# Optimization experiments

Measured on AMD Instinct MI355X. Metric: run time of the kernel, lower is better.

Reference implementation:

```python
import jax, jax.numpy as jnp
import numpy as np

M, P, B, TLEN = 512, 256, 128, 1024

def setup_inputs() -> dict:
    key = jax.random.key(0)
    k1, k2, k3, k4, k5, k6 = jax.random.split(key, 6)
    d_t = jax.random.normal(k1, (1, B, P), dtype=jnp.float32)
    s_t = jax.random.normal(k2, (1, B, P), dtype=jnp.float32)
    H = jax.random.normal(k3, (B, TLEN, M), dtype=jnp.float32)
    # torch.nn.Linear weights: shape [out_features, in_features]
    W_d = jax.random.normal(k4, (M, 2 * P), dtype=jnp.float32) / np.sqrt(2 * P)
    U_d = jax.random.normal(k5, (M, M), dtype=jnp.float32) / np.sqrt(M)
    v_d = jax.random.normal(k6, (1, M), dtype=jnp.float32) / np.sqrt(M)
    return {"d_t": d_t, "s_t": s_t, "H": H, "T": TLEN, "W_d": W_d, "U_d": U_d, "v_d": v_d}

def reference(d_t, s_t, H, T, W_d, U_d, v_d):
    # query: cat([d_t, s_t], dim=2) -> [1, B, 2p]; permute(1,0,2) -> [B, 1, 2p]
    query = jnp.concatenate([d_t, s_t], axis=2).transpose(1, 0, 2)  # [B, 1, 2p]
    # W_d(query) broadcast over T instead of materializing the repeat (same math)
    wq = jnp.einsum('boc,mc->bom', query, W_d)          # [B, 1, m]
    uh = jnp.einsum('btm,nm->btn', H, U_d)              # [B, T, m]
    beta = jnp.tanh(wq + uh)                            # [B, T, m]
    score = jnp.einsum('btm,om->bto', beta, v_d)        # [B, T, 1]
    score = score.transpose(0, 2, 1)                    # [B, 1, T]
    return jax.nn.softmax(score, axis=2)
```

## Files before the change

### kernel.cpp

```cpp
#include <hip/hip_runtime.h>
#include <hip/hip_bf16.h>
#include <stdint.h>

#define NB   128
#define NT   1024
#define NM   512
#define NP   256

typedef __attribute__((ext_vector_type(8))) short bf16x8;
typedef __attribute__((ext_vector_type(4))) float f32x4;
typedef unsigned int u32;

__device__ __forceinline__ uint32_t bfpair(float a, float b) {
    uint32_t ua = __float_as_uint(a) + 0x8000u;
    uint32_t ub = __float_as_uint(b) + 0x8000u;
    return __builtin_amdgcn_perm(ub, ua, 0x07060302u);
}

__device__ __forceinline__ bf16x8 pack8(float4 lo, float4 hi) {
    union { bf16x8 v; uint32_t u[4]; } r;
    r.u[0] = bfpair(lo.x, lo.y);
    r.u[1] = bfpair(lo.z, lo.w);
    r.u[2] = bfpair(hi.x, hi.y);
    r.u[3] = bfpair(hi.z, hi.w);
    return r.v;
}

__device__ __forceinline__ float fast_tanh(float x) {
    float e = __expf(2.0f * x);
    return 1.0f - 2.0f * __builtin_amdgcn_rcpf(e + 1.0f);
}

typedef const __attribute__((address_space(1))) u32* gas_t;
typedef __attribute__((address_space(3))) u32* las_t;
__device__ __forceinline__ void dma16(const void* g, void* l) {
    __builtin_amdgcn_global_load_lds((gas_t)g, (las_t)l, 16, 0, 0);
}

__global__ void prep_kernel(const float* __restrict__ U, unsigned short* __restrict__ Ub,
                            const float* __restrict__ d_t, const float* __restrict__ s_t,
                            const float* __restrict__ W, float* __restrict__ wq,
                            float* __restrict__ out) {
    const int bx = blockIdx.x;
    if (bx < 256) {
        int idx = bx * 256 + threadIdx.x;
        float4 u = reinterpret_cast<const float4*>(U)[idx];
        reinterpret_cast<uint2*>(Ub)[idx] = make_uint2(bfpair(u.x, u.y), bfpair(u.z, u.w));
    } else if (bx < 384) {
        int g = (bx - 256) * 512 + threadIdx.x * 2;
        int b = g >> 9;
        const float* dt = d_t + (size_t)b * NP;
        const float* st = s_t + (size_t)b * NP;
        #pragma unroll
        for (int e = 0; e < 2; ++e) {
            int n = (g + e) & 511;
            const float* Wn = W + (size_t)n * 512;
            float s = 0.f;
            #pragma unroll 4
            for (int c = 0; c < NP; c += 4) {
                float4 w0 = *reinterpret_cast<const float4*>(Wn + c);
                float4 q0 = *reinterpret_cast<const float4*>(dt + c);
                s += w0.x * q0.x + w0.y * q0.y + w0.z * q0.z + w0.w * q0.w;
                float4 w1 = *reinterpret_cast<const float4*>(Wn + NP + c);
                float4 q1 = *reinterpret_cast<const float4*>(st + c);
                s += w1.x * q1.x + w1.y * q1.y + w1.z * q1.z + w1.w * q1.w;
            }
            wq[g + e] = s;
        }
    } else {
        int idx = (bx - 384) * 256 + threadIdx.x;
        reinterpret_cast<float4*>(out)[idx] = make_float4(0.f, 0.f, 0.f, 0.f);
    }
}

__global__ __launch_bounds__(256, 2)
void score_kernel(const float* __restrict__ H, const unsigned short* __restrict__ Ub,
                  const float* __restrict__ wq, const float* __restrict__ v_d,
                  float* __restrict__ out) {
    __shared__ float          As[2][128 * 32];
    __shared__ unsigned short Bs[2][256 * 32];
    __shared__ float s_score[128];

    const int tid  = threadIdx.x;
    const int id   = blockIdx.x;
    const int tile = (id >> 4) * 8 + (id & 7);
    const int nh   = (id >> 3) & 1;
    const int tt   = tile & 7;
    const int b    = tile >> 3;

    const int lane = tid & 63;
    const int w    = tid >> 6;
    const int lr   = lane & 15;
    const int lq   = lane >> 4;
    const int tw   = w >> 1;
    const int nw   = w & 1;

    if (tid < 128) s_score[tid] = 0.f;

    const float* gA[4];
    const unsigned short* gB[4];
    unsigned lL[4];
    #pragma unroll
    for (int q = 0; q < 4; ++q) {
        int rA = w * 32 + q * 8 + (lane >> 3);
        int cA = (lane & 7) ^ (rA & 7);
        gA[q] = H + ((size_t)(b * NT + tt * 128 + rA)) * NM + cA * 4;
        int rB = w * 64 + q * 16 + (lane >> 2);
        int cB = (lane & 3) ^ ((rB >> 1) & 3);
        gB[q] = Ub + ((size_t)(nh * 256 + rB)) * NM + cB * 8;
        lL[q] = (unsigned)((w * 4 + q) * 1024 + lane * 16);
    }

    f32x4 acc[4][8];
    #pragma unroll
    for (int i = 0; i < 4; ++i)
        #pragma unroll
        for (int j = 0; j < 8; ++j)
            acc[i][j] = (f32x4){0.f, 0.f, 0.f, 0.f};

    #pragma unroll
    for (int q = 0; q < 4; ++q) dma16(gA[q], (char*)As[0] + lL[q]);
    #pragma unroll
    for (int q = 0; q < 4; ++q) dma16(gB[q], (char*)Bs[0] + lL[q]);

    #pragma unroll
    for (int kk = 0; kk < 16; ++kk) {
        const int cur = kk & 1;
        const int nxt = cur ^ 1;
        __syncthreads();
        if (kk < 15) {
            #pragma unroll
            for (int q = 0; q < 4; ++q) { gA[q] += 32; dma16(gA[q], (char*)As[nxt] + lL[q]); }
            #pragma unroll
            for (int q = 0; q < 4; ++q) { gB[q] += 32; dma16(gB[q], (char*)Bs[nxt] + lL[q]); }
        }

        bf16x8 a[4];
        #pragma unroll
        for (int i = 0; i < 4; ++i) {
            int t_loc = tw * 64 + i * 16 + lr;
            int s = t_loc & 7;
            const char* base = (const char*)As[cur] + t_loc * 128;
            float4 lo = *reinterpret_cast<const float4*>(base + (((2 * lq)     ^ s) * 16));
            float4 hi = *reinterpret_cast<const float4*>(base + (((2 * lq + 1) ^ s) * 16));
            a[i] = pack8(lo, hi);
        }
        bf16x8 bb[8];
        #pragma unroll
        for (int j = 0; j < 8; ++j) {
            int n_loc = nw * 128 + j * 16 + lr;
            int slot = lq ^ ((n_loc >> 1) & 3);
            bb[j] = *reinterpret_cast<const bf16x8*>((const char*)Bs[cur] + n_loc * 64 + slot * 16);
        }

        #pragma unroll
        for (int i = 0; i < 4; ++i)
            #pragma unroll
            for (int j = 0; j < 8; ++j)
                acc[i][j] = __builtin_amdgcn_mfma_f32_16x16x32_bf16(a[i], bb[j], acc[i][j], 0, 0, 0);
    }

    const float* wqb = wq + (size_t)b * NM;
    float vv[8], wv[8];
    #pragma unroll
    for (int j = 0; j < 8; ++j) {
        int n = nh * 256 + nw * 128 + j * 16 + lr;
        vv[j] = v_d[n];
        wv[j] = wqb[n];
    }
    #pragma unroll
    for (int i = 0; i < 4; ++i) {
        #pragma unroll
        for (int r = 0; r < 4; ++r) {
            float s = 0.f;
            #pragma unroll
            for (int j = 0; j < 8; ++j)
                s += vv[j] * fast_tanh(wv[j] + acc[i][j][r]);
            #pragma unroll
            for (int off = 1; off < 16; off <<= 1)
                s += __shfl_xor(s, off, 64);
            if (lr == 0) atomicAdd(&s_score[tw * 64 + i * 16 + lq * 4 + r], s);
        }
    }
    __syncthreads();
    if (tid < 128) atomicAdd(&out[(size_t)b * NT + tt * 128 + tid], s_score[tid]);
}

__global__ void softmax_kernel(float* __restrict__ out) {
    const int b   = blockIdx.x;
    const int tid = threadIdx.x;
    float* p = out + (size_t)b * NT;
    float4 v = reinterpret_cast<float4*>(p)[tid];
    float m = fmaxf(fmaxf(v.x, v.y), fmaxf(v.z, v.w));
    #pragma unroll
    for (int off = 32; off >= 1; off >>= 1)
        m = fmaxf(m, __shfl_xor(m, off, 64));
    __shared__ float red[8];
    const int wv = tid >> 6;
    if ((tid & 63) == 0) red[wv] = m;
    __syncthreads();
    m = fmaxf(fmaxf(red[0], red[1]), fmaxf(red[2], red[3]));
    float e0 = __expf(v.x - m), e1 = __expf(v.y - m);
    float e2 = __expf(v.z - m), e3 = __expf(v.w - m);
    float s = e0 + e1 + e2 + e3;
    #pragma unroll
    for (int off = 32; off >= 1; off >>= 1)
        s += __shfl_xor(s, off, 64);
    if ((tid & 63) == 0) red[4 + wv] = s;
    __syncthreads();
    s = red[4] + red[5] + red[6] + red[7];
    float inv = 1.f / s;
    float4 o;
    o.x = e0 * inv; o.y = e1 * inv; o.z = e2 * inv; o.w = e3 * inv;
    reinterpret_cast<float4*>(p)[tid] = o;
}

extern "C" void kernel_launch(void* const* d_in, const int* in_sizes, int n_in,
                              void* d_out, int out_size, void* d_ws, size_t ws_size,
                              hipStream_t stream) {
    const float* d_t = (const float*)d_in[0];
    const float* s_t = (const float*)d_in[1];
    const float* H   = (const float*)d_in[2];
    const float* W_d = (const float*)d_in[4];
    const float* U_d = (const float*)d_in[5];
    const float* v_d = (const float*)d_in[6];
    float* out = (float*)d_out;

    unsigned short* Ub = (unsigned short*)d_ws;
    float* wq = (float*)((char*)d_ws + 512 * 1024);

    prep_kernel<<<512, 256, 0, stream>>>(U_d, Ub, d_t, s_t, W_d, wq, out);
    score_kernel<<<2048, 256, 0, stream>>>(H, Ub, wq, v_d, out);
    softmax_kernel<<<NB, 256, 0, stream>>>(out);
}
```

Before: 467.8 us.

## Convert H to bf16 at LDS store and triple-buffer U tiles

The H tile is now loaded into registers, converted to bf16 once and written to LDS, replacing the fp32 DMA path where every wave re-read fp32 and re-packed it per MFMA. This halves the A-tile LDS footprint and read traffic. U tiles use a three-stage ring with prefetch two steps ahead and hand-placed vmcnt/lgkmcnt waits plus raw barriers. The cost is more VGPRs for in-flight H values and fragile manual waitcnt ordering.

```diff
diff --git a/kernel.cpp b/kernel.cpp
--- a/kernel.cpp
+++ b/kernel.cpp
@@ -15,15 +15,6 @@
     uint32_t ua = __float_as_uint(a) + 0x8000u;
     uint32_t ub = __float_as_uint(b) + 0x8000u;
     return __builtin_amdgcn_perm(ub, ua, 0x07060302u);
-}
-
-__device__ __forceinline__ bf16x8 pack8(float4 lo, float4 hi) {
-    union { bf16x8 v; uint32_t u[4]; } r;
-    r.u[0] = bfpair(lo.x, lo.y);
-    r.u[1] = bfpair(lo.z, lo.w);
-    r.u[2] = bfpair(hi.x, hi.y);
-    r.u[3] = bfpair(hi.z, hi.w);
-    return r.v;
 }
 
 __device__ __forceinline__ float fast_tanh(float x) {
@@ -77,8 +68,8 @@
 void score_kernel(const float* __restrict__ H, const unsigned short* __restrict__ Ub,
                   const float* __restrict__ wq, const float* __restrict__ v_d,
                   float* __restrict__ out) {
-    __shared__ float          As[2][128 * 32];
-    __shared__ unsigned short Bs[2][256 * 32];
+    __shared__ unsigned short As[2][128 * 32];
+    __shared__ unsigned short Bs[3][256 * 32];
     __shared__ float s_score[128];
 
     const int tid  = threadIdx.x;
@@ -98,18 +89,24 @@
     if (tid < 128) s_score[tid] = 0.f;
 
     const float* gA[4];
+    u32 woff[4];
+    #pragma unroll
+    for (int q = 0; q < 4; ++q) {
+        int r = w * 32 + q * 8 + (lane >> 3);
+        gA[q] = H + ((size_t)(b * NT + tt * 128 + r)) * NM + (lane & 7) * 4;
+        woff[q] = (u32)(r * 64 + ((((lane & 7) >> 1) ^ ((r >> 1) & 3)) << 4) + (lane & 1) * 8);
+    }
     const unsigned short* gB[4];
-    unsigned lL[4];
+    u32 lB[4];
     #pragma unroll
     for (int q = 0; q < 4; ++q) {
-        int rA = w * 32 + q * 8 + (lane >> 3);
-        int cA = (lane & 7) ^ (rA & 7);
-        gA[q] = H + ((size_t)(b * NT + tt * 128 + rA)) * NM + cA * 4;
         int rB = w * 64 + q * 16 + (lane >> 2);
         int cB = (lane & 3) ^ ((rB >> 1) & 3);
         gB[q] = Ub + ((size_t)(nh * 256 + rB)) * NM + cB * 8;
-        lL[q] = (unsigned)((w * 4 + q) * 1024 + lane * 16);
-    }
+        lB[q] = (u32)((w * 4 + q) * 1024 + lane * 16);
+    }
+    const u32 aro = (u32)((tw * 64 + lr) * 64 + ((lq ^ ((lr >> 1) & 3)) << 4));
+    const u32 bro = (u32)((nw * 128 + lr) * 64 + ((lq ^ ((lr >> 1) & 3)) << 4));
 
     f32x4 acc[4][8];
     #pragma unroll
@@ -118,46 +115,68 @@
         for (int j = 0; j < 8; ++j)
             acc[i][j] = (f32x4){0.f, 0.f, 0.f, 0.f};
 
-    #pragma unroll
-    for (int q = 0; q < 4; ++q) dma16(gA[q], (char*)As[0] + lL[q]);
-    #pragma unroll
-    for (int q = 0; q < 4; ++q) dma16(gB[q], (char*)Bs[0] + lL[q]);
+    float4 av[4];
+    #pragma unroll
+    for (int q = 0; q < 4; ++q) { av[q] = *reinterpret_cast<const float4*>(gA[q]); gA[q] += 32; }
+    #pragma unroll
+    for (int q = 0; q < 4; ++q) { dma16(gB[q], (char*)Bs[0] + lB[q]); gB[q] += 32; }
+    #pragma unroll
+    for (int q = 0; q < 4; ++q)
+        *reinterpret_cast<uint2*>((char*)As[0] + woff[q]) =
+            make_uint2(bfpair(av[q].x, av[q].y), bfpair(av[q].z, av[q].w));
+    #pragma unroll
+    for (int q = 0; q < 4; ++q) { av[q] = *reinterpret_cast<const float4*>(gA[q]); gA[q] += 32; }
+    #pragma unroll
+    for (int q = 0; q < 4; ++q) { dma16(gB[q], (char*)Bs[1] + lB[q]); gB[q] += 32; }
+
+    asm volatile("s_waitcnt vmcnt(8)" ::: "memory");
+    asm volatile("s_waitcnt lgkmcnt(0)" ::: "memory");
+    __builtin_amdgcn_s_barrier();
+    __builtin_amdgcn_sched_barrier(0);
 
     #pragma unroll
     for (int kk = 0; kk < 16; ++kk) {
-        const int cur = kk & 1;
-        const int nxt = cur ^ 1;
-        __syncthreads();
+        const char* ab = (const char*)As[kk & 1] + aro;
+        bf16x8 a0 = *reinterpret_cast<const bf16x8*>(ab);
+        bf16x8 a1 = *reinterpret_cast<const bf16x8*>(ab + 1024);
+        bf16x8 a2 = *reinterpret_cast<const bf16x8*>(ab + 2048);
+        bf16x8 a3 = *reinterpret_cast<const bf16x8*>(ab + 3072);
+
         if (kk < 15) {
-            #pragma unroll
-            for (int q = 0; q < 4; ++q) { gA[q] += 32; dma16(gA[q], (char*)As[nxt] + lL[q]); }
-            #pragma unroll
-            for (int q = 0; q < 4; ++q) { gB[q] += 32; dma16(gB[q], (char*)Bs[nxt] + lL[q]); }
-        }
-
-        bf16x8 a[4];
-        #pragma unroll
-        for (int i = 0; i < 4; ++i) {
-            int t_loc = tw * 64 + i * 16 + lr;
-            int s = t_loc & 7;
-            const char* base = (const char*)As[cur] + t_loc * 128;
-            float4 lo = *reinterpret_cast<const float4*>(base + (((2 * lq)     ^ s) * 16));
-            float4 hi = *reinterpret_cast<const float4*>(base + (((2 * lq + 1) ^ s) * 16));
-            a[i] = pack8(lo, hi);
-        }
-        bf16x8 bb[8];
+            char* an = (char*)As[(kk + 1) & 1];
+            #pragma unroll
+            for (int q = 0; q < 4; ++q)
+                *reinterpret_cast<uint2*>(an + woff[q]) =
+                    make_uint2(bfpair(av[q].x, av[q].y), bfpair(av[q].z, av[q].w));
+        }
+        if (kk < 14) {
+            #pragma unroll
+            for (int q = 0; q < 4; ++q) { av[q] = *reinterpret_cast<const float4*>(gA[q]); gA[q] += 32; }
+            char* bn = (char*)Bs[(kk + 2) % 3];
+            #pragma unroll
+            for (int q = 0; q < 4; ++q) { dma16(gB[q], bn + lB[q]); gB[q] += 32; }
+        }
+
+        const char* bbb = (const char*)Bs[kk % 3] + bro;
         #pragma unroll
         for (int j = 0; j < 8; ++j) {
-            int n_loc = nw * 128 + j * 16 + lr;
-            int slot = lq ^ ((n_loc >> 1) & 3);
-            bb[j] = *reinterpret_cast<const bf16x8*>((const char*)Bs[cur] + n_loc * 64 + slot * 16);
-        }
-
-        #pragma unroll
-        for (int i = 0; i < 4; ++i)
-            #pragma unroll
-            for (int j = 0; j < 8; ++j)
-                acc[i][j] = __builtin_amdgcn_mfma_f32_16x16x32_bf16(a[i], bb[j], acc[i][j], 0, 0, 0);
+            bf16x8 bbj = *reinterpret_cast<const bf16x8*>(bbb + j * 1024);
+            acc[0][j] = __builtin_amdgcn_mfma_f32_16x16x32_bf16(a0, bbj, acc[0][j], 0, 0, 0);
+            acc[1][j] = __builtin_amdgcn_mfma_f32_16x16x32_bf16(a1, bbj, acc[1][j], 0, 0, 0);
+            acc[2][j] = __builtin_amdgcn_mfma_f32_16x16x32_bf16(a2, bbj, acc[2][j], 0, 0, 0);
+            acc[3][j] = __builtin_amdgcn_mfma_f32_16x16x32_bf16(a3, bbj, acc[3][j], 0, 0, 0);
+        }
+
+        if (kk < 14) {
+            asm volatile("s_waitcnt vmcnt(8)" ::: "memory");
+        } else if (kk == 14) {
+            asm volatile("s_waitcnt vmcnt(0)" ::: "memory");
+        }
+        if (kk < 15) {
+            asm volatile("s_waitcnt lgkmcnt(0)" ::: "memory");
+            __builtin_amdgcn_s_barrier();
+            __builtin_amdgcn_sched_barrier(0);
+        }
     }
 
     const float* wqb = wq + (size_t)b * NM;
```

Measured after the change: 455.4 us. 2.7% less time.

## Restructure score kernel as persistent per-batch loop with register-resident U weights

Applied to the files above, without the earlier changes.

Each block now owns one batch and one half of the output features, keeping its slice of the bf16 U matrix in registers and looping over all time tiles. H is loaded into registers, converted to bf16 with a packed convert instruction, and written into a double-buffered LDS tile, with one barrier per k-step. This removes repeated U tile loads and per-use fp32-to-bf16 packing from LDS. In exchange it uses fewer, larger blocks with heavy register use, which risks low occupancy and latency exposure.

```diff
diff --git a/kernel.cpp b/kernel.cpp
--- a/kernel.cpp
+++ b/kernel.cpp
@@ -17,24 +17,15 @@
     return __builtin_amdgcn_perm(ub, ua, 0x07060302u);
 }
 
-__device__ __forceinline__ bf16x8 pack8(float4 lo, float4 hi) {
-    union { bf16x8 v; uint32_t u[4]; } r;
-    r.u[0] = bfpair(lo.x, lo.y);
-    r.u[1] = bfpair(lo.z, lo.w);
-    r.u[2] = bfpair(hi.x, hi.y);
-    r.u[3] = bfpair(hi.z, hi.w);
-    return r.v;
+__device__ __forceinline__ u32 cvtpk(float lo, float hi) {
+    u32 d;
+    asm("v_cvt_pk_bf16_f32 %0, %1, %2" : "=v"(d) : "v"(lo), "v"(hi));
+    return d;
 }
 
 __device__ __forceinline__ float fast_tanh(float x) {
     float e = __expf(2.0f * x);
     return 1.0f - 2.0f * __builtin_amdgcn_rcpf(e + 1.0f);
-}
-
-typedef const __attribute__((address_space(1))) u32* gas_t;
-typedef __attribute__((address_space(3))) u32* las_t;
-__device__ __forceinline__ void dma16(const void* g, void* l) {
-    __builtin_amdgcn_global_load_lds((gas_t)g, (las_t)l, 16, 0, 0);
 }
 
 __global__ void prep_kernel(const float* __restrict__ U, unsigned short* __restrict__ Ub,
@@ -73,117 +64,139 @@
     }
 }
 
-__global__ __launch_bounds__(256, 2)
+__global__ __launch_bounds__(512, 2)
 void score_kernel(const float* __restrict__ H, const unsigned short* __restrict__ Ub,
                   const float* __restrict__ wq, const float* __restrict__ v_d,
                   float* __restrict__ out) {
-    __shared__ float          As[2][128 * 32];
-    __shared__ unsigned short Bs[2][256 * 32];
-    __shared__ float s_score[128];
+    __shared__ __align__(16) unsigned char smem[16384 + 64 * 9 * 4];
+    char* AsB = (char*)smem;
+    float* redf = (float*)(smem + 16384);
 
     const int tid  = threadIdx.x;
     const int id   = blockIdx.x;
-    const int tile = (id >> 4) * 8 + (id & 7);
+    const int b    = (id & 7) + ((id >> 4) << 3);
     const int nh   = (id >> 3) & 1;
-    const int tt   = tile & 7;
-    const int b    = tile >> 3;
 
     const int lane = tid & 63;
     const int w    = tid >> 6;
     const int lr   = lane & 15;
     const int lq   = lane >> 4;
-    const int tw   = w >> 1;
-    const int nw   = w & 1;
-
-    if (tid < 128) s_score[tid] = 0.f;
-
-    const float* gA[4];
-    const unsigned short* gB[4];
-    unsigned lL[4];
+
+    bf16x8 Bf[2][16];
+    {
+        const unsigned short* gb = Ub + (size_t)(nh * 256 + w * 32 + lr) * NM + lq * 8;
+        #pragma unroll
+        for (int nf = 0; nf < 2; ++nf)
+            #pragma unroll
+            for (int kf = 0; kf < 16; ++kf)
+                Bf[nf][kf] = *reinterpret_cast<const bf16x8*>(gb + nf * 16 * NM + kf * 32);
+    }
+
+    const int rowA = tid >> 3, seg = tid & 7;
+    const float* gAt = H + (size_t)b * NT * NM + (size_t)rowA * NM + seg * 8;
+    const u32 woff = (u32)(rowA * 128 + ((seg ^ (rowA & 7)) << 4));
+
+    const u32 aoB = (u32)(lr * 128 + ((lq ^ (lr & 7)) << 4));
+
+    float vv[2], wvq[2];
+    {
+        const int nb0 = nh * 256 + w * 32 + lr;
+        vv[0]  = v_d[nb0];            vv[1]  = v_d[nb0 + 16];
+        wvq[0] = wq[b * NM + nb0];    wvq[1] = wq[b * NM + nb0 + 16];
+    }
+
+    f32x4 acc[4][2];
     #pragma unroll
-    for (int q = 0; q < 4; ++q) {
-        int rA = w * 32 + q * 8 + (lane >> 3);
-        int cA = (lane & 7) ^ (rA & 7);
-        gA[q] = H + ((size_t)(b * NT + tt * 128 + rA)) * NM + cA * 4;
-        int rB = w * 64 + q * 16 + (lane >> 2);
-        int cB = (lane & 3) ^ ((rB >> 1) & 3);
-        gB[q] = Ub + ((size_t)(nh * 256 + rB)) * NM + cB * 8;
-        lL[q] = (unsigned)((w * 4 + q) * 1024 + lane * 16);
-    }
-
-    f32x4 acc[4][8];
-    #pragma unroll
-    for (int i = 0; i < 4; ++i)
-        #pragma unroll
-        for (int j = 0; j < 8; ++j)
-            acc[i][j] = (f32x4){0.f, 0.f, 0.f, 0.f};
-
-    #pragma unroll
-    for (int q = 0; q < 4; ++q) dma16(gA[q], (char*)As[0] + lL[q]);
-    #pragma unroll
-    for (int q = 0; q < 4; ++q) dma16(gB[q], (char*)Bs[0] + lL[q]);
-
-    #pragma unroll
-    for (int kk = 0; kk < 16; ++kk) {
-        const int cur = kk & 1;
-        const int nxt = cur ^ 1;
-        __syncthreads();
-        if (kk < 15) {
-            #pragma unroll
-            for (int q = 0; q < 4; ++q) { gA[q] += 32; dma16(gA[q], (char*)As[nxt] + lL[q]); }
-            #pragma unroll
-            for (int q = 0; q < 4; ++q) { gB[q] += 32; dma16(gB[q], (char*)Bs[nxt] + lL[q]); }
-        }
-
-        bf16x8 a[4];
-        #pragma unroll
-        for (int i = 0; i < 4; ++i) {
-            int t_loc = tw * 64 + i * 16 + lr;
-            int s = t_loc & 7;
-            const char* base = (const char*)As[cur] + t_loc * 128;
-            float4 lo = *reinterpret_cast<const float4*>(base + (((2 * lq)     ^ s) * 16));
-            float4 hi = *reinterpret_cast<const float4*>(base + (((2 * lq + 1) ^ s) * 16));
-            a[i] = pack8(lo, hi);
-        }
-        bf16x8 bb[8];
-        #pragma unroll
-        for (int j = 0; j < 8; ++j) {
-            int n_loc = nw * 128 + j * 16 + lr;
-            int slot = lq ^ ((n_loc >> 1) & 3);
-            bb[j] = *reinterpret_cast<const bf16x8*>((const char*)Bs[cur] + n_loc * 64 + slot * 16);
-        }
-
-        #pragma unroll
-        for (int i = 0; i < 4; ++i)
-            #pragma unroll
-            for (int j = 0; j < 8; ++j)
-                acc[i][j] = __builtin_amdgcn_mfma_f32_16x16x32_bf16(a[i], bb[j], acc[i][j], 0, 0, 0);
-    }
-
-    const float* wqb = wq + (size_t)b * NM;
-    float vv[8], wv[8];
-    #pragma unroll
-    for (int j = 0; j < 8; ++j) {
-        int n = nh * 256 + nw * 128 + j * 16 + lr;
-        vv[j] = v_d[n];
-        wv[j] = wqb[n];
-    }
-    #pragma unroll
-    for (int i = 0; i < 4; ++i) {
-        #pragma unroll
-        for (int r = 0; r < 4; ++r) {
-            float s = 0.f;
-            #pragma unroll
-            for (int j = 0; j < 8; ++j)
-                s += vv[j] * fast_tanh(wv[j] + acc[i][j][r]);
-            #pragma unroll
-            for (int off = 1; off < 16; off <<= 1)
-                s += __shfl_xor(s, off, 64);
-            if (lr == 0) atomicAdd(&s_score[tw * 64 + i * 16 + lq * 4 + r], s);
-        }
-    }
-    __syncthreads();
-    if (tid < 128) atomicAdd(&out[(size_t)b * NT + tt * 128 + tid], s_score[tid]);
+    for (int i = 0; i < 4; ++i) { acc[i][0] = (f32x4){0,0,0,0}; acc[i][1] = (f32x4){0,0,0,0}; }
+
+    float4 av[2][2];
+    av[0][0] = *reinterpret_cast<const float4*>(gAt);
+    av[0][1] = *reinterpret_cast<const float4*>(gAt + 4);
+    av[1][0] = *reinterpret_cast<const float4*>(gAt + 64);
+    av[1][1] = *reinterpret_cast<const float4*>(gAt + 64 + 4);
+    {
+        uint4 wv4;
+        wv4.x = cvtpk(av[0][0].x, av[0][0].y); wv4.y = cvtpk(av[0][0].z, av[0][0].w);
+        wv4.z = cvtpk(av[0][1].x, av[0][1].y); wv4.w = cvtpk(av[0][1].z, av[0][1].w);
+        *reinterpret_cast<uint4*>(AsB + woff) = wv4;
+    }
+    asm volatile("s_waitcnt lgkmcnt(0)" ::: "memory");
+    __builtin_amdgcn_s_barrier();
+    __builtin_amdgcn_sched_barrier(0);
+
+    float* outb = out + (size_t)b * NT;
+
+    #pragma unroll 1
+    for (int tt = 0; tt < 16; ++tt) {
+        const float* gAtn = (tt < 15) ? (gAt + 64 * NM) : gAt;
+
+        #pragma unroll
+        for (int s = 0; s < 8; ++s) {
+            const char* rb = AsB + (s & 1) * 8192;
+
+            bf16x8 a[4][2];
+            #pragma unroll
+            for (int tf = 0; tf < 4; ++tf)
+                #pragma unroll
+                for (int kf = 0; kf < 2; ++kf)
+                    a[tf][kf] = *reinterpret_cast<const bf16x8*>(
+                        rb + ((aoB ^ (u32)(kf << 6)) + tf * 2048));
+
+            {
+                const float* ga = (s < 6) ? (gAt + (s + 2) * 64)
+                                          : (gAtn + (s - 6) * 64);
+                av[s & 1][0] = *reinterpret_cast<const float4*>(ga);
+                av[s & 1][1] = *reinterpret_cast<const float4*>(ga + 4);
+            }
+
+            #pragma unroll
+            for (int tf = 0; tf < 4; ++tf)
+                #pragma unroll
+                for (int nf = 0; nf < 2; ++nf)
+                    #pragma unroll
+                    for (int kf = 0; kf < 2; ++kf)
+                        acc[tf][nf] = __builtin_amdgcn_mfma_f32_16x16x32_bf16(
+                            a[tf][kf], Bf[nf][(s & 7) * 2 + kf], acc[tf][nf], 0, 0, 0);
+
+            {
+                float4 A0 = av[(s + 1) & 1][0], A1 = av[(s + 1) & 1][1];
+                uint4 wv4;
+                wv4.x = cvtpk(A0.x, A0.y); wv4.y = cvtpk(A0.z, A0.w);
+                wv4.z = cvtpk(A1.x, A1.y); wv4.w = cvtpk(A1.z, A1.w);
+                *reinterpret_cast<uint4*>(AsB + (((s + 1) & 1) * 8192) + woff) = wv4;
+            }
+
+            asm volatile("s_waitcnt lgkmcnt(0)" ::: "memory");
+            __builtin_amdgcn_s_barrier();
+            __builtin_amdgcn_sched_barrier(0);
+        }
+
+        #pragma unroll
+        for (int tf = 0; tf < 4; ++tf) {
+            #pragma unroll
+            for (int r = 0; r < 4; ++r) {
+                float sv = vv[0] * fast_tanh(wvq[0] + acc[tf][0][r])
+                         + vv[1] * fast_tanh(wvq[1] + acc[tf][1][r]);
+                sv += __shfl_xor(sv, 1, 64);
+                sv += __shfl_xor(sv, 2, 64);
+                sv += __shfl_xor(sv, 4, 64);
+                sv += __shfl_xor(sv, 8, 64);
+                if (lr == 0) redf[(tf * 16 + lq * 4 + r) * 9 + w] = sv;
+            }
+            acc[tf][0] = (f32x4){0, 0, 0, 0};
+            acc[tf][1] = (f32x4){0, 0, 0, 0};
+        }
+        asm volatile("s_waitcnt lgkmcnt(0)" ::: "memory");
+        __builtin_amdgcn_s_barrier();
+        __builtin_amdgcn_sched_barrier(0);
+        if (tid < 64) {
+            const float* rp = redf + tid * 9;
+            float s = ((rp[0] + rp[1]) + (rp[2] + rp[3]))
+                    + ((rp[4] + rp[5]) + (rp[6] + rp[7]));
+            atomicAdd(&outb[tt * 64 + tid], s);
+        }
+        gAt += 64 * NM;
+    }
 }
 
 __global__ void softmax_kernel(float* __restrict__ out) {
@@ -230,6 +243,6 @@
     float* wq = (float*)((char*)d_ws + 512 * 1024);
 
     prep_kernel<<<512, 256, 0, stream>>>(U_d, Ub, d_t, s_t, W_d, wq, out);
-    score_kernel<<<2048, 256, 0, stream>>>(H, Ub, wq, v_d, out);
+    score_kernel<<<256, 512, 0, stream>>>(H, Ub, wq, v_d, out);
     softmax_kernel<<<NB, 256, 0, stream>>>(out);
 }
```

Result: no change. 474.2 us (+1.4%).
